# Kernel optimization log

Hardware: AMD Instinct MI355X
Metric: run time of the kernel (lower is better)

Reference implementation:

```python
import jax, jax.numpy as jnp
import numpy as np
from jax import lax

# Static model/config sizes
B, ANG, C, H, NF, NB = 1, 9, 3, 128, 16, 2


def get_freq_position(n):
    """Anti-diagonal frequency bands of an n x n angular-DCT grid (python/static)."""
    bands = []
    for i in range(n):
        bands.append(([i], [0]))
    for j in range(1, n):
        bands.append(([n - 1], [j]))
    for item in bands:
        while item[0][0] > 0 and item[1][0] < n - 1:
            item[0].insert(0, item[0][0] - 1)
            item[1].insert(0, item[1][0] + 1)
    return bands


def dct_mat(n):
    """Orthonormal DCT-II matrix (row k = k-th basis)."""
    k = jnp.arange(n, dtype=jnp.float32)[:, None]
    i = jnp.arange(n, dtype=jnp.float32)[None, :]
    m = jnp.cos(jnp.pi * (i + 0.5) * k / n) * jnp.sqrt(2.0 / n)
    return m.at[0].multiply(1.0 / np.sqrt(2.0))


def conv3d(x, w, b):
    # x: (N, Cin, D, H, W), w: (Cout, Cin, 3, 3, 3)
    y = lax.conv_general_dilated(x, w, (1, 1, 1), 'SAME',
                                 dimension_numbers=('NCDHW', 'OIDHW', 'NCDHW'))
    return y + b[None, :, None, None, None]


def branch(cut, wi, bi, a, wb, bb):
    """init conv + NB ResBlock3D (PReLU -> Conv3d, residual), plus outer skip."""
    y0 = conv3d(cut, wi, bi)
    y = y0
    for k in range(NB):
        r = jnp.where(y >= 0, y, a[k] * y)  # PReLU (single-parameter)
        y = y + conv3d(r, wb[k], bb[k])
    return y0 + y


def setup_inputs() -> dict:
    key = jax.random.key(0)
    ks = jax.random.split(key, 32)

    def nrm(k, shape, s=0.05):
        return jax.random.normal(k, shape, dtype=jnp.float32) * s

    inp = {"x": jax.random.normal(ks[0], (B, ANG, ANG, C, H, H), dtype=jnp.float32)}
    i = 1
    for n in ("dc", "lo", "mi", "hi"):
        inp[f"w_{n}_i"] = nrm(ks[i], (NF, C, 3, 3, 3)); i += 1
        inp[f"b_{n}_i"] = nrm(ks[i], (NF,)); i += 1
        inp[f"a_{n}"] = jnp.full((NB,), 0.25, dtype=jnp.float32)
        inp[f"w_{n}"] = nrm(ks[i], (NB, NF, NF, 3, 3, 3)); i += 1
        inp[f"b_{n}"] = nrm(ks[i], (NB, NF)); i += 1
    inp["w_last"] = nrm(ks[i], (C, NF))  # 1x1 Conv2d, no bias
    return inp


def reference(x, w_dc_i, b_dc_i, a_dc, w_dc, b_dc,
              w_lo_i, b_lo_i, a_lo, w_lo, b_lo,
              w_mi_i, b_mi_i, a_mi, w_mi, b_mi,
              w_hi_i, b_hi_i, a_hi, w_hi, b_hi, w_last):
    b, u, v, c, h, w = x.shape
    Da = dct_mat(u)  # angular DCT (u == v)
    Ds = dct_mat(h)  # spatial DCT (h == w)

    # SpaAngDCT: spatial 2D DCT then angular 2D DCT
    xf = jnp.einsum('buvchw,Hh,Ww->buvcHW', x, Ds, Ds)
    xf = jnp.einsum('buvchw,Uu,Vv->bUVchw', xf, Da, Da)

    x_rec = jnp.zeros((b, NF, u, v, h, w), dtype=x.dtype)
    for idx, (ui, vi) in enumerate(get_freq_position(u)):
        if idx == 0:
            p = (w_dc_i, b_dc_i, a_dc, w_dc, b_dc)
        elif idx <= 2:
            p = (w_lo_i, b_lo_i, a_lo, w_lo, b_lo)
        elif idx <= u - 1:
            p = (w_mi_i, b_mi_i, a_mi, w_mi, b_mi)
        else:
            p = (w_hi_i, b_hi_i, a_hi, w_hi, b_hi)
        ua, va = jnp.array(ui), jnp.array(vi)
        cut = xf[:, ua, va].transpose(0, 2, 1, 3, 4)  # (b, c, L, h, w)
        out = branch(cut, *p)                          # (b, NF, L, h, w)
        x_rec = x_rec.at[:, :, ua, va].set(out)        # scatter band back

    # 'b c u v h w -> b c (u h) (v w)' then 1x1 conv (NF -> 3)
    xr = x_rec.transpose(0, 1, 2, 4, 3, 5).reshape(b, NF, u * h, v * w)
    xr = jnp.einsum('bnHW,on->boHW', xr, w_last)
    xr = xr.reshape(b, c, u, h, v, w).transpose(0, 2, 4, 1, 3, 5)  # (b,u,v,c,h,w)

    # InverseSpaAngDCT: angular IDCT then spatial IDCT
    xr = jnp.einsum('bUVchw,Uu,Vv->buvchw', xr, Da, Da)
    xr = jnp.einsum('buvcHW,Hh,Ww->buvchw', xr, Ds, Ds)
    return xr + x
```

## Files before the change

### kernel.cpp

```cpp
#include <hip/hip_runtime.h>
#include <hip/hip_bf16.h>
#include <math.h>

typedef __hip_bfloat16 bf16;
typedef __attribute__((ext_vector_type(8))) short short8;
typedef __attribute__((ext_vector_type(4))) float floatx4;
typedef __attribute__((ext_vector_type(4))) unsigned int uint4v;
typedef __attribute__((ext_vector_type(2))) unsigned int uint2v;

#define HW 16384
#define NSLICE 243

__constant__ int c_s_of_p[81] = {
  0, 1,1, 2,2,2, 3,3,3,3, 4,4,4,4,4, 5,5,5,5,5,5, 6,6,6,6,6,6,6,
  7,7,7,7,7,7,7,7, 8,8,8,8,8,8,8,8,8, 9,9,9,9,9,9,9,9,
  10,10,10,10,10,10,10, 11,11,11,11,11,11, 12,12,12,12,12,
  13,13,13,13, 14,14,14, 15,15, 16};
__constant__ int c_l_of_p[81] = {
  0, 0,1, 0,1,2, 0,1,2,3, 0,1,2,3,4, 0,1,2,3,4,5, 0,1,2,3,4,5,6,
  0,1,2,3,4,5,6,7, 0,1,2,3,4,5,6,7,8, 0,1,2,3,4,5,6,7,
  0,1,2,3,4,5,6, 0,1,2,3,4,5, 0,1,2,3,4, 0,1,2,3, 0,1,2, 0,1, 0};
__constant__ int c_L_of_s[17] = {1,2,3,4,5,6,7,8,9,8,7,6,5,4,3,2,1};
__constant__ int c_g_of_s[17] = {0,1,1,2,2,2,2,2,2,3,3,3,3,3,3,3,3};
__constant__ int c_pos_uv[81] = {
  0,1,3,6,10,15,21,28,36,
  2,4,7,11,16,22,29,37,45,
  5,8,12,17,23,30,38,46,53,
  9,13,18,24,31,39,47,54,60,
  14,19,25,32,40,48,55,61,66,
  20,26,33,41,49,56,62,67,71,
  27,34,42,50,57,63,68,72,75,
  35,43,51,58,64,69,73,76,78,
  44,52,59,65,70,74,77,79,80};

struct WPtrs {
  const float* wi[4]; const float* bi[4]; const float* a[4];
  const float* wb[4]; const float* bb[4]; const float* wl;
};

__device__ __forceinline__ unsigned short f2bf(float f) {
  return __bfloat16_as_ushort(__float2bfloat16(f));
}
__device__ __forceinline__ float bf2f(unsigned short u) {
  return __uint_as_float(((unsigned int)u) << 16);
}
__device__ __forceinline__ float bflo(unsigned int w) {
  return __uint_as_float(w << 16);
}
__device__ __forceinline__ float bfhi(unsigned int w) {
  return __uint_as_float(w & 0xffff0000u);
}
__device__ __forceinline__ unsigned int pack2(float a, float b) {
  return (unsigned int)f2bf(a) | ((unsigned int)f2bf(b) << 16);
}
__device__ __forceinline__ float invprelu(float v, float invA) {
  return (v >= 0.f) ? v : v * invA;
}
__device__ __forceinline__ void bfsplit(float v, unsigned short& hi, unsigned short& lo) {
  unsigned int bits = __float_as_uint(v);
  hi = (unsigned short)(bits >> 16);
  lo = f2bf(v - __uint_as_float(bits & 0xffff0000u));
}
__device__ __forceinline__ void gl_lds16(const void* g, void* l) {
  __builtin_amdgcn_global_load_lds(
      (const __attribute__((address_space(1))) unsigned int*)g,
      (__attribute__((address_space(3))) unsigned int*)l, 16, 0, 0);
}
__device__ __forceinline__ int ldsoff(int plane, int col) {
  return plane * 2112 + ((plane & 3) << 5) + (col << 4);
}

__global__ __launch_bounds__(256) void k_init(WPtrs P, float* DaF,
                                              unsigned short* TFhi, unsigned short* TFlo,
                                              unsigned short* TIhi, unsigned short* TIlo,
                                              unsigned short* Wmf,
                                              float* BiF, float* BbF,
                                              float* AF, float* WlF) {
  const double PI = 3.14159265358979323846;
  int t = blockIdx.x * 256 + threadIdx.x;
  if (t < 81) {
    int U = t / 9, u = t % 9;
    double d = cos(PI * (u + 0.5) * U / 9.0) * sqrt(2.0 / 9.0);
    if (U == 0) d *= (1.0 / sqrt(2.0));
    DaF[t] = (float)d;
  }
  if (t < 16384) {
    int jj = t & 7, lane = (t >> 3) & 63, ks = (t >> 9) & 3, tile = t >> 11;
    int row = tile * 16 + (lane & 15);
    int colk = ks * 32 + (lane >> 4) * 8 + jj;
    double vF = cos(PI * (colk + 0.5) * row / 128.0) * sqrt(2.0 / 128.0);
    if (row == 0) vF *= (1.0 / sqrt(2.0));
    double vI = cos(PI * (row + 0.5) * colk / 128.0) * sqrt(2.0 / 128.0);
    if (colk == 0) vI *= (1.0 / sqrt(2.0));
    unsigned short h, l;
    bfsplit((float)vF, h, l); TFhi[t] = h; TFlo[t] = l;
    bfsplit((float)vI, h, l); TIhi[t] = h; TIlo[t] = l;
  }
  if (t < 92160) {
    int s = t / 7680, r = t % 7680;
    int step = r / 512, r2 = r % 512;
    int lane = r2 >> 3, j = r2 & 7;
    int d = step / 5, i = step % 5;
    int q = lane >> 4, m = lane & 15;
    int tl = 2 * i + (q >> 1);
    int cin = (q & 1) * 8 + j;
    float val = 0.f;
    if (tl <= 8) {
      int ky = tl / 3, kx = tl % 3;
      int tap = d * 9 + ky * 3 + kx;
      if (s < 4) {
        if (cin < 3) val = P.wi[s][(m * 3 + cin) * 27 + tap];
      } else {
        int g = (s - 4) >> 1, k = (s - 4) & 1;
        val = P.wb[g][((k * 16 + m) * 16 + cin) * 27 + tap];
      }
    }
    Wmf[t] = f2bf(val);
  }
  if (t < 64)  BiF[t] = P.bi[t / 16][t % 16];
  if (t < 128) BbF[t] = P.bb[t / 32][t % 32];
  if (t < 8)   AF[t]  = P.a[t / 2][t % 2];
  if (t < 48)  WlF[t] = P.wl[t];
}

__global__ __launch_bounds__(1024) void k_dct2(const float* __restrict__ X,
                                               const unsigned short* __restrict__ tabhi,
                                               const unsigned short* __restrict__ tablo,
                                               const float* __restrict__ xres,
                                               float* __restrict__ Yf,
                                               unsigned short* __restrict__ Ybf) {
  __shared__ unsigned short sThi[128 * 136];
  __shared__ unsigned short sTlo[128 * 136];
  int s = blockIdx.x;
  int t = threadIdx.x;
  int lane = t & 63, wv16 = t >> 6;
  int mt8 = wv16 & 7, nh = wv16 >> 3;
  int q = lane >> 4, n16 = lane & 15;
  const float* Xs = X + (size_t)s * HW;

  floatx4 acc[4];
#pragma unroll
  for (int ntl = 0; ntl < 4; ntl++) acc[ntl] = (floatx4){0.f, 0.f, 0.f, 0.f};

#pragma unroll
  for (int ks = 0; ks < 4; ks++) {
    short8 ahi, alo;
    {
      const float* xp = Xs + (mt8 * 16 + n16) * 128 + ks * 32 + q * 8;
      float4 a = *(const float4*)xp;
      float4 b = *(const float4*)(xp + 4);
      union { short8 v; unsigned short u[8]; } H, L;
      float xv[8] = {a.x, a.y, a.z, a.w, b.x, b.y, b.z, b.w};
#pragma unroll
      for (int j = 0; j < 8; j++) bfsplit(xv[j], H.u[j], L.u[j]);
      ahi = H.v; alo = L.v;
    }
#pragma unroll
    for (int ntl = 0; ntl < 4; ntl++) {
      int e = (nh * 4 + ntl) * 2048 + ks * 512 + lane * 8;
      short8 bh = *(const short8*)(tabhi + e);
      short8 bl = *(const short8*)(tablo + e);
      acc[ntl] = __builtin_amdgcn_mfma_f32_16x16x32_bf16(ahi, bl, acc[ntl], 0, 0, 0);
      acc[ntl] = __builtin_amdgcn_mfma_f32_16x16x32_bf16(alo, bh, acc[ntl], 0, 0, 0);
      acc[ntl] = __builtin_amdgcn_mfma_f32_16x16x32_bf16(ahi, bh, acc[ntl], 0, 0, 0);
    }
  }

#pragma unroll
  for (int ntl = 0; ntl < 4; ntl++) {
    int col = (nh * 4 + ntl) * 16 + n16;
    int rowb = mt8 * 16 + q * 4;
#pragma unroll
    for (int rp = 0; rp < 4; rp += 2) {
      unsigned short h0, l0, h1, l1;
      bfsplit(acc[ntl][rp], h0, l0);
      bfsplit(acc[ntl][rp + 1], h1, l1);
      int widx = (col * 136 + rowb + rp) >> 1;
      ((unsigned int*)sThi)[widx] = (unsigned int)h0 | ((unsigned int)h1 << 16);
      ((unsigned int*)sTlo)[widx] = (unsigned int)l0 | ((unsigned int)l1 << 16);
    }
  }
  __syncthreads();

#pragma unroll
  for (int ntl = 0; ntl < 4; ntl++) acc[ntl] = (floatx4){0.f, 0.f, 0.f, 0.f};

#pragma unroll
  for (int ks = 0; ks < 4; ks++) {
    int e0 = mt8 * 2048 + ks * 512 + lane * 8;
    short8 ahi = *(const short8*)(tabhi + e0);
    short8 alo = *(const short8*)(tablo + e0);
#pragma unroll
    for (int ntl = 0; ntl < 4; ntl++) {
      int off = ((nh * 4 + ntl) * 16 + n16) * 136 + ks * 32 + q * 8;
      short8 bh = *(const short8*)(sThi + off);
      short8 bl = *(const short8*)(sTlo + off);
      acc[ntl] = __builtin_amdgcn_mfma_f32_16x16x32_bf16(ahi, bl, acc[ntl], 0, 0, 0);
      acc[ntl] = __builtin_amdgcn_mfma_f32_16x16x32_bf16(alo, bh, acc[ntl], 0, 0, 0);
      acc[ntl] = __builtin_amdgcn_mfma_f32_16x16x32_bf16(ahi, bh, acc[ntl], 0, 0, 0);
    }
  }

#pragma unroll
  for (int ntl = 0; ntl < 4; ntl++) {
    int row0 = mt8 * 16 + q * 4;
    int col = (nh * 4 + ntl) * 16 + n16;
#pragma unroll
    for (int r = 0; r < 4; r++) {
      size_t oi = (size_t)s * HW + (size_t)(row0 + r) * 128 + col;
      float v = acc[ntl][r];
      if (Ybf) {
        Ybf[oi] = f2bf(v);
      } else {
        if (xres) v += xres[oi];
        Yf[oi] = v;
      }
    }
  }
}

__global__ __launch_bounds__(256) void k_angfwd(const unsigned short* __restrict__ in,
                                                const float* __restrict__ DaF,
                                                unsigned short* __restrict__ out) {
  __shared__ float sDa[81];
  int t = threadIdx.x;
  if (t < 81) sDa[t] = DaF[t];
  __syncthreads();
  int idx = blockIdx.x * 256 + t;
  int hw = idx & (HW - 1);
  int r = idx >> 14;
  int c = r % 3, ub = r / 3;
  unsigned short raw[81];
#pragma unroll
  for (int u = 0; u < 9; u++)
#pragma unroll
    for (int v = 0; v < 9; v++)
      raw[u * 9 + v] = in[(size_t)((u * 9 + v) * 3 + c) * HW + hw];
  float tmp[3][9];
#pragma unroll
  for (int i = 0; i < 3; i++)
#pragma unroll
    for (int v = 0; v < 9; v++) tmp[i][v] = 0.f;
#pragma unroll
  for (int u = 0; u < 9; u++) {
    float fv[9];
#pragma unroll
    for (int v = 0; v < 9; v++) fv[v] = bf2f(raw[u * 9 + v]);
#pragma unroll
    for (int i = 0; i < 3; i++) {
      float dc = sDa[(ub * 3 + i) * 9 + u];
#pragma unroll
      for (int v = 0; v < 9; v++) tmp[i][v] += dc * fv[v];
    }
  }
#pragma unroll
  for (int i = 0; i < 3; i++) {
    int U = ub * 3 + i;
#pragma unroll
    for (int V = 0; V < 9; V++) {
      float acc = 0.f;
#pragma unroll
      for (int v = 0; v < 9; v++) acc += sDa[V * 9 + v] * tmp[i][v];
      size_t base = ((size_t)c_pos_uv[U * 9 + V] * HW + hw) * 4;
      out[base + c] = f2bf(acc);
      if (c == 0) out[base + 3] = 0;
    }
  }
}

__global__ __launch_bounds__(256) void k_anginv(const float* __restrict__ xrb,
                                                const float* __restrict__ DaF,
                                                float* __restrict__ out) {
  __shared__ float sDa[81];
  int t = threadIdx.x;
  if (t < 81) sDa[t] = DaF[t];
  __syncthreads();
  int idx = blockIdx.x * 256 + t;
  int hw = idx & (HW - 1);
  int r = idx >> 14;
  int c = r % 3, ub = r / 3;
  float raw[81];
#pragma unroll
  for (int U = 0; U < 9; U++)
#pragma unroll
    for (int V = 0; V < 9; V++)
      raw[U * 9 + V] = xrb[((size_t)c_pos_uv[U * 9 + V] * 3 + c) * HW + hw];
  float tmp[3][9];
#pragma unroll
  for (int i = 0; i < 3; i++)
#pragma unroll
    for (int V = 0; V < 9; V++) tmp[i][V] = 0.f;
#pragma unroll
  for (int U = 0; U < 9; U++) {
#pragma unroll
    for (int i = 0; i < 3; i++) {
      float dc = sDa[U * 9 + (ub * 3 + i)];
#pragma unroll
      for (int V = 0; V < 9; V++) tmp[i][V] += dc * raw[U * 9 + V];
    }
  }
#pragma unroll
  for (int i = 0; i < 3; i++) {
    int u = ub * 3 + i;
#pragma unroll
    for (int v = 0; v < 9; v++) {
      float acc = 0.f;
#pragma unroll
      for (int V = 0; V < 9; V++) acc += sDa[V * 9 + v] * tmp[i][V];
      out[(size_t)((u * 9 + v) * 3 + c) * HW + hw] = acc;
    }
  }
}

__global__ __launch_bounds__(1024, 8) void k_conv(const unsigned short* __restrict__ src,
                                              const unsigned short* __restrict__ prevAct,
                                              const unsigned short* __restrict__ act0,
                                              const unsigned short* __restrict__ Wmf,
                                              const float* __restrict__ BiF,
                                              const float* __restrict__ BbF,
                                              const float* __restrict__ AF,
                                              const float* __restrict__ WlF,
                                              int sel,
                                              unsigned short* __restrict__ boutAct,
                                              float* __restrict__ xrbOut) {
  __shared__ unsigned short s_lds[21184];
  int p = blockIdx.y;
  int s = c_s_of_p[p], l = c_l_of_p[p];
  int g = c_g_of_s[s], Ls = c_L_of_s[s];
  int row0 = blockIdx.x * 8;
  int t = threadIdx.x;
  int lane = t & 63, wv16 = t >> 6;
  int row8 = wv16 & 7, ch = wv16 >> 3;
  int q = lane >> 4, n = lane & 15;

  float aNext = (sel < 2) ? AF[g * 2 + sel] : 0.f;
  float invA  = (sel > 0) ? 1.0f / AF[g * 2 + sel - 1] : 0.f;

  {
    uint4v z = (uint4v){0u, 0u, 0u, 0u};
    int zmax = (sel == 0) ? 1320 : 40;
    for (int i = t; i < zmax; i += 1024) {
      int row, half, col;
      if (i < 40) { row = i >> 2; half = (i >> 1) & 1; col = (i & 1) ? 129 : 0; }
      else { int j = i - 40; row = j >> 7; col = (j & 127) + 1; half = 1; }
      *(uint4v*)((char*)s_lds + ldsoff(row * 2 + half, col)) = z;
    }
    for (int row = 0; row < 10; row++) {
      int grow = row0 - 1 + row;
      if ((unsigned)grow >= 128u) {
        for (int i = t; i < 264; i += 1024) {
          int half = i / 132, col = i % 132;
          *(uint4v*)((char*)s_lds + ldsoff(row * 2 + half, col)) = z;
        }
      }
    }
  }

  int off2[5];
#pragma unroll
  for (int i = 0; i < 5; i++) {
    int tl = 2 * i + (q >> 1);
    if (tl > 8) tl = 8;
    int ky = tl / 3, kx = tl % 3;
    off2[i] = ldsoff(2 * (row8 + ky) + (q & 1), n + kx) + ch * 1024;
  }

  int setIdx = (sel == 0) ? g : (4 + g * 2 + (sel - 1));
  const char* WsetBase = (const char*)Wmf + (size_t)setIdx * 15 * 1024;

  floatx4 acc[4];
#pragma unroll
  for (int cg = 0; cg < 4; cg++) acc[cg] = (floatx4){0.f, 0.f, 0.f, 0.f};

  for (int d = 0; d < 3; d++) {
    int l2 = l + d - 1;
    if (l2 < 0 || l2 >= Ls) continue;
    int p2 = p + d - 1;
    __syncthreads();
    if (sel == 0) {
#pragma unroll
      for (int it = 0; it < 2; it++) {
        int id = t + it * 1024;
        if (id < 1280) {
          int row = id >> 7, col = id & 127;
          int grow = row0 - 1 + row;
          if ((unsigned)grow < 128u) {
            uint2v w = *(const uint2v*)(src +
                ((size_t)p2 * HW + (size_t)grow * 128 + col) * 4);
            uint4v val; val.x = w.x; val.y = w.y; val.z = 0u; val.w = 0u;
            *(uint4v*)((char*)s_lds + ldsoff(row * 2, col + 1)) = val;
          }
        }
      }
    } else {
#pragma unroll
      for (int it = 0; it < 3; it++) {
        int id = t + it * 1024;
        if (id < 2560) {
          int row = id >> 8, half = (id >> 7) & 1, col = id & 127;
          int grow = row0 - 1 + row;
          if ((unsigned)grow < 128u) {
            const void* gp = (const void*)(src +
                (((size_t)p2 * HW + (size_t)grow * 128 + col) * 16 + half * 8));
            void* lp = (void*)((char*)s_lds + ldsoff(row * 2 + half, col + 1));
            gl_lds16(gp, lp);
          }
        }
      }
    }
    __syncthreads();
    short8 af[5];
#pragma unroll
    for (int i = 0; i < 5; i++)
      af[i] = *(const short8*)(WsetBase + ((d * 5 + i) * 64 + lane) * 16);
#pragma unroll
    for (int cg = 0; cg < 4; cg++) {
#pragma unroll
      for (int i = 0; i < 5; i++) {
        short8 b = *(const short8*)((const char*)s_lds + off2[i] + cg * 256);
        acc[cg] = __builtin_amdgcn_mfma_f32_16x16x32_bf16(af[i], b, acc[cg], 0, 0, 0);
      }
    }
  }

  const float* bp = (sel == 0) ? (BiF + g * 16) : (BbF + g * 32 + (sel - 1) * 16);
  float bz[4];
#pragma unroll
  for (int r = 0; r < 4; r++) bz[r] = bp[q * 4 + r];
  int h = row0 + row8;

  if (sel < 2) {
#pragma unroll
    for (int cg = 0; cg < 4; cg++) {
      size_t pix = (size_t)p * HW + h * 128 + ch * 64 + cg * 16 + n;
      float r0 = acc[cg][0] + bz[0], r1 = acc[cg][1] + bz[1];
      float r2 = acc[cg][2] + bz[2], r3 = acc[cg][3] + bz[3];
      if (sel != 0) {
        uint2v pv = *(const uint2v*)(prevAct + pix * 16 + q * 4);
        r0 += invprelu(bflo(pv.x), invA); r1 += invprelu(bfhi(pv.x), invA);
        r2 += invprelu(bflo(pv.y), invA); r3 += invprelu(bfhi(pv.y), invA);
      }
      r0 = fmaxf(r0, 0.f) + aNext * fminf(r0, 0.f);
      r1 = fmaxf(r1, 0.f) + aNext * fminf(r1, 0.f);
      r2 = fmaxf(r2, 0.f) + aNext * fminf(r2, 0.f);
      r3 = fmaxf(r3, 0.f) + aNext * fminf(r3, 0.f);
      uint2v ov; ov.x = pack2(r0, r1); ov.y = pack2(r2, r3);
      *(uint2v*)(boutAct + pix * 16 + q * 4) = ov;
    }
  } else {
    float invA0 = 1.0f / AF[g * 2];
    float wl0[4], wl1[4], wl2[4];
#pragma unroll
    for (int r = 0; r < 4; r++) {
      wl0[r] = WlF[q * 4 + r];
      wl1[r] = WlF[16 + q * 4 + r];
      wl2[r] = WlF[32 + q * 4 + r];
    }
#pragma unroll
    for (int cg = 0; cg < 4; cg++) {
      size_t pix = (size_t)p * HW + h * 128 + ch * 64 + cg * 16 + n;
      float r0 = acc[cg][0] + bz[0], r1 = acc[cg][1] + bz[1];
      float r2 = acc[cg][2] + bz[2], r3 = acc[cg][3] + bz[3];
      uint2v pv = *(const uint2v*)(prevAct + pix * 16 + q * 4);
      r0 += invprelu(bflo(pv.x), invA); r1 += invprelu(bfhi(pv.x), invA);
      r2 += invprelu(bflo(pv.y), invA); r3 += invprelu(bfhi(pv.y), invA);
      uint2v p0 = *(const uint2v*)(act0 + pix * 16 + q * 4);
      r0 += invprelu(bflo(p0.x), invA0); r1 += invprelu(bfhi(p0.x), invA0);
      r2 += invprelu(bflo(p0.y), invA0); r3 += invprelu(bfhi(p0.y), invA0);
      float o0 = wl0[0] * r0 + wl0[1] * r1 + wl0[2] * r2 + wl0[3] * r3;
      float o1 = wl1[0] * r0 + wl1[1] * r1 + wl1[2] * r2 + wl1[3] * r3;
      float o2 = wl2[0] * r0 + wl2[1] * r1 + wl2[2] * r2 + wl2[3] * r3;
      o0 += __shfl_xor(o0, 16); o0 += __shfl_xor(o0, 32);
      o1 += __shfl_xor(o1, 16); o1 += __shfl_xor(o1, 32);
      o2 += __shfl_xor(o2, 16); o2 += __shfl_xor(o2, 32);
      if (q == 0) {
        size_t hw = (size_t)h * 128 + ch * 64 + cg * 16 + n;
        xrbOut[((size_t)p * 3 + 0) * HW + hw] = o0;
        xrbOut[((size_t)p * 3 + 1) * HW + hw] = o1;
        xrbOut[((size_t)p * 3 + 2) * HW + hw] = o2;
      }
    }
  }
}

extern "C" void kernel_launch(void* const* d_in, const int* in_sizes, int n_in,
                              void* d_out, int out_size, void* d_ws, size_t ws_size,
                              hipStream_t stream) {
  (void)in_sizes; (void)n_in; (void)out_size; (void)ws_size;
  const float* x = (const float*)d_in[0];
  WPtrs P;
  for (int g = 0; g < 4; g++) {
    int b = 1 + g * 5;
    P.wi[g] = (const float*)d_in[b + 0];
    P.bi[g] = (const float*)d_in[b + 1];
    P.a[g]  = (const float*)d_in[b + 2];
    P.wb[g] = (const float*)d_in[b + 3];
    P.bb[g] = (const float*)d_in[b + 4];
  }
  P.wl = (const float*)d_in[21];

  char* base = (char*)d_ws;
  size_t off = 0;
  auto take = [&](size_t bytes) -> char* {
    char* r = base + off;
    off += (bytes + 255) & ~(size_t)255;
    return r;
  };
  float* DaF = (float*)take(81 * 4);
  unsigned short* TFhi = (unsigned short*)take(16384 * 2);
  unsigned short* TFlo = (unsigned short*)take(16384 * 2);
  unsigned short* TIhi = (unsigned short*)take(16384 * 2);
  unsigned short* TIlo = (unsigned short*)take(16384 * 2);
  unsigned short* Wmf = (unsigned short*)take(92160 * 2);
  float* BiF   = (float*)take(256);
  float* BbF   = (float*)take(512);
  float* AF    = (float*)take(32);
  float* WlF   = (float*)take(192);
  float* R1 = (float*)take((size_t)NSLICE * HW * 4);
  unsigned short* B1 = (unsigned short*)take((size_t)NSLICE * HW * 2);
  float* R3 = (float*)take((size_t)NSLICE * HW * 4);
  unsigned short* braw0 = (unsigned short*)take((size_t)81 * 16 * HW * 2);
  unsigned short* braw1 = (unsigned short*)take((size_t)81 * 16 * HW * 2);
  unsigned short* xf2b = (unsigned short*)R3;
  float* xrb = R3;

  k_init<<<360, 256, 0, stream>>>(P, DaF, TFhi, TFlo, TIhi, TIlo,
                                  Wmf, BiF, BbF, AF, WlF);
  k_dct2<<<243, 1024, 0, stream>>>(x, TFhi, TFlo, nullptr, nullptr, B1);
  k_angfwd<<<576, 256, 0, stream>>>(B1, DaF, xf2b);
  k_conv<<<dim3(16, 81), 1024, 0, stream>>>(xf2b, nullptr, nullptr, Wmf,
                                            BiF, BbF, AF, WlF, 0, braw0, nullptr);
  k_conv<<<dim3(16, 81), 1024, 0, stream>>>(braw0, braw0, nullptr, Wmf,
                                            BiF, BbF, AF, WlF, 1, braw1, nullptr);
  k_conv<<<dim3(16, 81), 1024, 0, stream>>>(braw1, braw1, braw0, Wmf,
                                            BiF, BbF, AF, WlF, 2, nullptr, xrb);
  k_anginv<<<576, 256, 0, stream>>>(xrb, DaF, R1);
  k_dct2<<<243, 1024, 0, stream>>>(R1, TIhi, TIlo, x, (float*)d_out, nullptr);
}
```

Baseline: 267.8 us.

## Fold weight repack into DCT launch, read residual from LDS, reorder depth taps

The weight repacking moves out of k_init into extra blocks of the first k_dct2 launch, so k_init shrinks to 64 blocks and the repack runs alongside the DCT. The conv epilogue now reads the previous activation from the already-staged LDS tile instead of global memory. The conv depth loop visits taps in the order 0,2,1, and the angular forward kernel writes channel 2 plus the zero padding with a single 32-bit store. The LDS read relies on the centre depth plane still being in LDS after the last iteration, which is why the depth order changed; this is a correctness dependency to watch.

```diff
diff --git a/kernel.cpp b/kernel.cpp
--- a/kernel.cpp
+++ b/kernel.cpp
@@ -69,11 +69,32 @@
 __device__ __forceinline__ int ldsoff(int plane, int col) {
   return plane * 2112 + ((plane & 3) << 5) + (col << 4);
 }
+__device__ __forceinline__ void wmf_repack(const WPtrs& P, unsigned short* Wmf, int t) {
+  if (t >= 92160) return;
+  int s = t / 7680, r = t % 7680;
+  int step = r / 512, r2 = r % 512;
+  int lane = r2 >> 3, j = r2 & 7;
+  int d = step / 5, i = step % 5;
+  int q = lane >> 4, m = lane & 15;
+  int tl = 2 * i + (q >> 1);
+  int cin = (q & 1) * 8 + j;
+  float val = 0.f;
+  if (tl <= 8) {
+    int ky = tl / 3, kx = tl % 3;
+    int tap = d * 9 + ky * 3 + kx;
+    if (s < 4) {
+      if (cin < 3) val = P.wi[s][(m * 3 + cin) * 27 + tap];
+    } else {
+      int g = (s - 4) >> 1, k = (s - 4) & 1;
+      val = P.wb[g][((k * 16 + m) * 16 + cin) * 27 + tap];
+    }
+  }
+  Wmf[t] = f2bf(val);
+}
 
 __global__ __launch_bounds__(256) void k_init(WPtrs P, float* DaF,
                                               unsigned short* TFhi, unsigned short* TFlo,
                                               unsigned short* TIhi, unsigned short* TIlo,
-                                              unsigned short* Wmf,
                                               float* BiF, float* BbF,
                                               float* AF, float* WlF) {
   const double PI = 3.14159265358979323846;
@@ -96,27 +117,6 @@
     bfsplit((float)vF, h, l); TFhi[t] = h; TFlo[t] = l;
     bfsplit((float)vI, h, l); TIhi[t] = h; TIlo[t] = l;
   }
-  if (t < 92160) {
-    int s = t / 7680, r = t % 7680;
-    int step = r / 512, r2 = r % 512;
-    int lane = r2 >> 3, j = r2 & 7;
-    int d = step / 5, i = step % 5;
-    int q = lane >> 4, m = lane & 15;
-    int tl = 2 * i + (q >> 1);
-    int cin = (q & 1) * 8 + j;
-    float val = 0.f;
-    if (tl <= 8) {
-      int ky = tl / 3, kx = tl % 3;
-      int tap = d * 9 + ky * 3 + kx;
-      if (s < 4) {
-        if (cin < 3) val = P.wi[s][(m * 3 + cin) * 27 + tap];
-      } else {
-        int g = (s - 4) >> 1, k = (s - 4) & 1;
-        val = P.wb[g][((k * 16 + m) * 16 + cin) * 27 + tap];
-      }
-    }
-    Wmf[t] = f2bf(val);
-  }
   if (t < 64)  BiF[t] = P.bi[t / 16][t % 16];
   if (t < 128) BbF[t] = P.bb[t / 32][t % 32];
   if (t < 8)   AF[t]  = P.a[t / 2][t % 2];
@@ -128,7 +128,14 @@
                                                const unsigned short* __restrict__ tablo,
                                                const float* __restrict__ xres,
                                                float* __restrict__ Yf,
-                                               unsigned short* __restrict__ Ybf) {
+                                               unsigned short* __restrict__ Ybf,
+                                               WPtrs P,
+                                               unsigned short* __restrict__ Wmf) {
+  if (blockIdx.x >= 243) {
+    int t2 = (blockIdx.x - 243) * 1024 + threadIdx.x;
+    wmf_repack(P, Wmf, t2);
+    return;
+  }
   __shared__ unsigned short sThi[128 * 136];
   __shared__ unsigned short sTlo[128 * 136];
   int s = blockIdx.x;
@@ -262,8 +269,11 @@
 #pragma unroll
       for (int v = 0; v < 9; v++) acc += sDa[V * 9 + v] * tmp[i][v];
       size_t base = ((size_t)c_pos_uv[U * 9 + V] * HW + hw) * 4;
-      out[base + c] = f2bf(acc);
-      if (c == 0) out[base + 3] = 0;
+      if (c == 2) {
+        *(unsigned int*)(out + base + 2) = (unsigned int)f2bf(acc);
+      } else {
+        out[base + c] = f2bf(acc);
+      }
     }
   }
 }
@@ -372,7 +382,9 @@
 #pragma unroll
   for (int cg = 0; cg < 4; cg++) acc[cg] = (floatx4){0.f, 0.f, 0.f, 0.f};
 
-  for (int d = 0; d < 3; d++) {
+  const int dord[3] = {0, 2, 1};
+  for (int k = 0; k < 3; k++) {
+    int d = dord[k];
     int l2 = l + d - 1;
     if (l2 < 0 || l2 >= Ls) continue;
     int p2 = p + d - 1;
@@ -436,7 +448,8 @@
       float r0 = acc[cg][0] + bz[0], r1 = acc[cg][1] + bz[1];
       float r2 = acc[cg][2] + bz[2], r3 = acc[cg][3] + bz[3];
       if (sel != 0) {
-        uint2v pv = *(const uint2v*)(prevAct + pix * 16 + q * 4);
+        uint2v pv = *(const uint2v*)((const char*)s_lds +
+            ldsoff(2 * (row8 + 1) + (q >> 1), ch * 64 + cg * 16 + n + 1) + (q & 1) * 8);
         r0 += invprelu(bflo(pv.x), invA); r1 += invprelu(bfhi(pv.x), invA);
         r2 += invprelu(bflo(pv.y), invA); r3 += invprelu(bfhi(pv.y), invA);
       }
@@ -461,7 +474,8 @@
       size_t pix = (size_t)p * HW + h * 128 + ch * 64 + cg * 16 + n;
       float r0 = acc[cg][0] + bz[0], r1 = acc[cg][1] + bz[1];
       float r2 = acc[cg][2] + bz[2], r3 = acc[cg][3] + bz[3];
-      uint2v pv = *(const uint2v*)(prevAct + pix * 16 + q * 4);
+      uint2v pv = *(const uint2v*)((const char*)s_lds +
+          ldsoff(2 * (row8 + 1) + (q >> 1), ch * 64 + cg * 16 + n + 1) + (q & 1) * 8);
       r0 += invprelu(bflo(pv.x), invA); r1 += invprelu(bfhi(pv.x), invA);
       r2 += invprelu(bflo(pv.y), invA); r3 += invprelu(bfhi(pv.y), invA);
       uint2v p0 = *(const uint2v*)(act0 + pix * 16 + q * 4);
@@ -524,9 +538,9 @@
   unsigned short* xf2b = (unsigned short*)R3;
   float* xrb = R3;
 
-  k_init<<<360, 256, 0, stream>>>(P, DaF, TFhi, TFlo, TIhi, TIlo,
-                                  Wmf, BiF, BbF, AF, WlF);
-  k_dct2<<<243, 1024, 0, stream>>>(x, TFhi, TFlo, nullptr, nullptr, B1);
+  k_init<<<64, 256, 0, stream>>>(P, DaF, TFhi, TFlo, TIhi, TIlo,
+                                 BiF, BbF, AF, WlF);
+  k_dct2<<<333, 1024, 0, stream>>>(x, TFhi, TFlo, nullptr, nullptr, B1, P, Wmf);
   k_angfwd<<<576, 256, 0, stream>>>(B1, DaF, xf2b);
   k_conv<<<dim3(16, 81), 1024, 0, stream>>>(xf2b, nullptr, nullptr, Wmf,
                                             BiF, BbF, AF, WlF, 0, braw0, nullptr);
@@ -535,5 +549,5 @@
   k_conv<<<dim3(16, 81), 1024, 0, stream>>>(braw1, braw1, braw0, Wmf,
                                             BiF, BbF, AF, WlF, 2, nullptr, xrb);
   k_anginv<<<576, 256, 0, stream>>>(xrb, DaF, R1);
-  k_dct2<<<243, 1024, 0, stream>>>(R1, TIhi, TIlo, x, (float*)d_out, nullptr);
-}
+  k_dct2<<<243, 1024, 0, stream>>>(R1, TIhi, TIlo, x, (float*)d_out, nullptr, P, Wmf);
+}
```

New measurement: 265.6 us. No clear change (-0.8%).
